# Optimization experiments

Measured on AMD Instinct MI355X. Metric: run time of the kernel, lower is better.

## Reference

```python
import jax, jax.numpy as jnp
import numpy as np

E = 8        # num_experts (material buckets)
L1 = 3072    # input dim
L2 = 15
L3 = 32
RF = 32      # ROUTER_FEATURES_PER_PERSPECTIVE
B = 16384
AUX_ALPHA = 0.01
Z_ALPHA = 0.001
LOAD_FLOOR = 0.05
LOAD_CAP = 0.5
PROBE_ALPHA = 0.01
PROBE_TAU = 1.0
PROBE_THRESH = 0.05
TEACHER_ALPHA = 0.0   # initial value of _teacher_alpha buffer
SCORE_SCALE = 600.0
SQ_SCALE = 255.0 / 256.0


def setup_inputs() -> dict:
    key = jax.random.key(0)
    ks = jax.random.split(key, 12)
    x = jax.random.uniform(ks[0], (B, L1), dtype=jnp.float32)
    ls_indices = jax.random.randint(ks[1], (B,), 0, E)
    psqt = jax.random.normal(ks[2], (B,), dtype=jnp.float32)
    score_target = jax.random.normal(ks[3], (B,), dtype=jnp.float32)
    router_w = 0.1 * jax.random.normal(ks[4], (E, 2 * RF), dtype=jnp.float32)
    router_b = jnp.zeros((E,), dtype=jnp.float32)
    # effective (coalesced) expert params, per _expert_params view
    w1 = jax.random.normal(ks[5], (E, L2 + 1, L1), dtype=jnp.float32) / np.sqrt(L1)
    b1 = 0.01 * jax.random.normal(ks[6], (E, L2 + 1), dtype=jnp.float32)
    w2 = jax.random.normal(ks[7], (E, L3, 2 * L2), dtype=jnp.float32) / np.sqrt(2 * L2)
    b2 = 0.01 * jax.random.normal(ks[8], (E, L3), dtype=jnp.float32)
    w3 = jax.random.normal(ks[9], (E, 1, L3), dtype=jnp.float32) / np.sqrt(L3)
    b3 = jnp.zeros((E, 1), dtype=jnp.float32)  # output bias zeroed in __init__
    return {"x": x, "ls_indices": ls_indices, "psqt": psqt,
            "score_target": score_target, "router_w": router_w,
            "router_b": router_b, "w1": w1, "b1": b1, "w2": w2, "b2": b2,
            "w3": w3, "b3": b3}


def _forward(x, psqt, score_target, router_w, router_b, w1, b1, w2, b2, w3, b3, ls_indices):
    half = L1 // 2
    router_in = jnp.concatenate([x[:, :RF], x[:, half:half + RF]], axis=1)  # [B, 64]
    gate_logits = router_in @ router_w.T + router_b                          # [B, E]
    logp = jax.nn.log_softmax(gate_logits, axis=-1)
    gate_probs = jnp.exp(logp)
    expert_indices = jnp.argmax(gate_logits, axis=-1)                        # [B]

    teacher_ce = -jnp.mean(jnp.take_along_axis(logp, ls_indices[:, None], axis=1))
    frac = jnp.bincount(expert_indices, length=E).astype(gate_probs.dtype) / gate_probs.shape[0]
    avg_gate = gate_probs.mean(axis=0)
    load = avg_gate + jax.lax.stop_gradient(frac - avg_gate)
    floor_loss = jnp.mean(jnp.square(jnp.maximum(LOAD_FLOOR - load, 0.0)))
    cap_loss = jnp.mean(jnp.square(jnp.maximum(load - LOAD_CAP, 0.0)))
    aux_loss = floor_loss + cap_loss
    z_loss = jnp.mean(jnp.square(jax.nn.logsumexp(gate_logits, axis=-1)))

    # ---- all-experts stacked MLP (fusion target) ----
    l1c = jnp.einsum('bi,eoi->beo', x, w1) + b1          # [B, E, L2+1]
    a, a_skip = l1c[..., :L2], l1c[..., L2:]              # [B,E,L2], [B,E,1]
    h = jnp.clip(jnp.concatenate([a * a * SQ_SCALE, a], axis=-1), 0.0, 1.0)  # [B,E,2*L2]
    l2x = jnp.clip(jnp.einsum('bei,eoi->beo', h, w2) + b2, 0.0, 1.0)         # [B,E,L3]
    all_out = jnp.einsum('bei,eoi->beo', l2x, w3) + b3 + a_skip              # [B,E,1]

    # ---- probe loss ----
    probe_weight = PROBE_ALPHA * max(PROBE_THRESH - TEACHER_ALPHA, 0.0) / max(PROBE_THRESH, 1e-9)
    expert_out = (all_out[..., 0] + psqt[:, None]) * SCORE_SCALE             # [B, E]
    err = jnp.square(expert_out - score_target[:, None])
    err = err - err.min(axis=1, keepdims=True)
    pt = jax.nn.softmax(-jax.lax.stop_gradient(err) / PROBE_TAU, axis=-1)
    log_pt = jnp.log(jnp.maximum(pt, 1e-30))
    probe_loss = jnp.mean(jnp.sum(pt * (log_pt - logp), axis=-1))            # kl_div batchmean

    router_loss = (AUX_ALPHA * aux_loss + Z_ALPHA * z_loss
                   + TEACHER_ALPHA * teacher_ce + probe_weight * probe_loss)

    l3x = jnp.take_along_axis(all_out, expert_indices[:, None, None], axis=1)[:, 0, :]  # [B, 1]
    gp = jnp.take_along_axis(gate_probs, expert_indices[:, None], axis=1)               # [B, 1]
    l3x = l3x * (1.0 + gp - jax.lax.stop_gradient(gp))  # straight-through (training mode)
    return l3x, router_loss


def reference(x, ls_indices, psqt, score_target, router_w, router_b, w1, b1, w2, b2, w3, b3):
    return _forward(x, psqt, score_target, router_w, router_b, w1, b1, w2, b2, w3, b3, ls_indices)
```

## Files before the change

### kernel.cpp

```cpp
#include <hip/hip_runtime.h>
#include <math.h>

#define BATCH 16384
#define K_DIM 3072
#define NEXP  8

typedef float  f32x4  __attribute__((ext_vector_type(4)));
typedef __bf16 bf16x8 __attribute__((ext_vector_type(8)));
typedef unsigned int u32x4 __attribute__((ext_vector_type(4)));
typedef unsigned int u32x2 __attribute__((ext_vector_type(2)));

__device__ __forceinline__ unsigned short f2bf(float f) {
  union { float f; unsigned u; } v; v.f = f;
  unsigned u = v.u + 0x7fffu + ((v.u >> 16) & 1u);
  return (unsigned short)(u >> 16);
}

__global__ void cvt_kernel(const float* __restrict__ w1, unsigned short* __restrict__ o,
                           const float* __restrict__ w2, float* __restrict__ w2t) {
  if (blockIdx.x < 384) {
    int i = blockIdx.x * 256 + threadIdx.x;
    f32x4 v = ((const f32x4*)w1)[i];
    u32x2 p = { (unsigned)f2bf(v.x) | ((unsigned)f2bf(v.y) << 16),
                (unsigned)f2bf(v.z) | ((unsigned)f2bf(v.w) << 16) };
    ((u32x2*)o)[i] = p;
  } else {
    for (int j = threadIdx.x; j < 7680; j += 256) {
      int e = j / 960; int r = j - e * 960; int oo = r / 30; int ii = r - oo * 30;
      w2t[e * 960 + ii * 32 + oo] = w2[j];
    }
  }
}

__global__ __launch_bounds__(256, 3) void moe_main_kernel(
    const float* __restrict__ x, const unsigned short* __restrict__ w1bf,
    const float* __restrict__ b1, const float* __restrict__ w2t,
    const float* __restrict__ b2, const float* __restrict__ w3,
    const float* __restrict__ b3, const float* __restrict__ psqt,
    const float* __restrict__ st, const float* __restrict__ rw,
    const float* __restrict__ rb, float* __restrict__ out,
    float* __restrict__ accs) {
  __shared__ __align__(16) unsigned short stage[32 * 72 + 128 * 72];
  __shared__ float rws_s[512];
  __shared__ float logps[32][8];
  __shared__ int   eidx_s[32];
  __shared__ int   hist_s[8];
  __shared__ float zsum_s;
  __shared__ float wred[4];

  const int tid = threadIdx.x;
  const int bm  = blockIdx.x;
  unsigned short* xs  = stage;
  unsigned short* wsd = stage + 32 * 72;
  float* Cl = (float*)stage;

  const int lane = tid & 63, wv = tid >> 6;
  const int l16 = lane & 15, lq = lane >> 4;
  const int rt = wv & 1;
  const int cb = (wv >> 1) * 4;

  const int xr0 = tid >> 4, xc4 = tid & 15;
  const float* gx0 = x + (size_t)(bm * 32 + xr0) * K_DIM + xc4 * 4;
  const float* gx1 = gx0 + (size_t)16 * K_DIM;
  const int xo0 = xr0 * 72 + xc4 * 4;
  const int xo1 = (xr0 + 16) * 72 + xc4 * 4;
  const int wr0 = tid >> 3, wc8 = tid & 7;
  const unsigned short* gw = w1bf + (size_t)wr0 * K_DIM + wc8 * 8;
  const int wo0 = wr0 * 72 + wc8 * 8;

  f32x4 xv0 = *(const f32x4*)gx0;
  f32x4 xv1 = *(const f32x4*)gx1;
  u32x4 wv0 = *(const u32x4*)(gw);
  u32x4 wv1 = *(const u32x4*)(gw + 32 * K_DIM);
  u32x4 wv2 = *(const u32x4*)(gw + 64 * K_DIM);
  u32x4 wv3 = *(const u32x4*)(gw + 96 * K_DIM);

  rws_s[tid] = rw[tid];
  rws_s[tid + 256] = rw[tid + 256];
  if (tid < 8) hist_s[tid] = 0;
  if (tid == 0) zsum_s = 0.f;
  __syncthreads();

  {
    const int rrow = tid >> 3, re = tid & 7;
    const float* xrow = x + (size_t)(bm * 32 + rrow) * K_DIM;
    double l = (double)rb[re];
#pragma unroll
    for (int c = 0; c < 32; ++c)
      l = fma((double)xrow[c], (double)rws_s[re * 64 + c], l);
#pragma unroll
    for (int c = 0; c < 32; ++c)
      l = fma((double)xrow[1536 + c], (double)rws_s[re * 64 + 32 + c], l);
    double mx = l;
    mx = fmax(mx, __shfl_xor(mx, 1));
    mx = fmax(mx, __shfl_xor(mx, 2));
    mx = fmax(mx, __shfl_xor(mx, 4));
    int cand = (l == mx) ? re : 8;
    cand = min(cand, __shfl_xor(cand, 1));
    cand = min(cand, __shfl_xor(cand, 2));
    cand = min(cand, __shfl_xor(cand, 4));
    double s = exp(l - mx);
    s += __shfl_xor(s, 1); s += __shfl_xor(s, 2); s += __shfl_xor(s, 4);
    double lse = mx + log(s);
    logps[rrow][re] = (float)(l - lse);
    if (re == 0) {
      eidx_s[rrow] = cand;
      atomicAdd(&zsum_s, (float)(lse * lse));
    }
    if (re == cand) atomicAdd(&hist_s[cand], 1);
  }

  f32x4 acc[4];
#pragma unroll
  for (int c = 0; c < 4; ++c) acc[c] = (f32x4){0.f, 0.f, 0.f, 0.f};

  const int abase = (rt * 16 + l16) * 72 + lq * 8;
  const int bbase = (cb * 16 + l16) * 72 + lq * 8;

  for (int kt = 0; kt < 48; ++kt) {
    __syncthreads();
    {
      u32x2 p0 = { (unsigned)f2bf(xv0.x) | ((unsigned)f2bf(xv0.y) << 16),
                   (unsigned)f2bf(xv0.z) | ((unsigned)f2bf(xv0.w) << 16) };
      *(u32x2*)&xs[xo0] = p0;
      u32x2 p1 = { (unsigned)f2bf(xv1.x) | ((unsigned)f2bf(xv1.y) << 16),
                   (unsigned)f2bf(xv1.z) | ((unsigned)f2bf(xv1.w) << 16) };
      *(u32x2*)&xs[xo1] = p1;
      *(u32x4*)&wsd[wo0]           = wv0;
      *(u32x4*)&wsd[wo0 + 32 * 72] = wv1;
      *(u32x4*)&wsd[wo0 + 64 * 72] = wv2;
      *(u32x4*)&wsd[wo0 + 96 * 72] = wv3;
    }
    __syncthreads();
    if (kt < 47) {
      gx0 += 64; gx1 += 64;
      xv0 = *(const f32x4*)gx0;
      xv1 = *(const f32x4*)gx1;
      const unsigned short* g = gw + (kt + 1) * 64;
      wv0 = *(const u32x4*)(g);
      wv1 = *(const u32x4*)(g + 32 * K_DIM);
      wv2 = *(const u32x4*)(g + 64 * K_DIM);
      wv3 = *(const u32x4*)(g + 96 * K_DIM);
    }
#pragma unroll
    for (int ks = 0; ks < 2; ++ks) {
      bf16x8 af = *(const bf16x8*)&xs[abase + ks * 32];
#pragma unroll
      for (int c = 0; c < 4; ++c) {
        bf16x8 bfv = *(const bf16x8*)&wsd[bbase + c * 16 * 72 + ks * 32];
        acc[c] = __builtin_amdgcn_mfma_f32_16x16x32_bf16(af, bfv, acc[c], 0, 0, 0);
      }
    }
  }

  __syncthreads();
#pragma unroll
  for (int c = 0; c < 4; ++c)
#pragma unroll
    for (int r = 0; r < 4; ++r)
      Cl[(rt * 16 + lq * 4 + r) * 132 + (cb + c) * 16 + l16] = acc[c][r];
  __syncthreads();

  const int bl = tid >> 3, e = tid & 7;
  const int bg = bm * 32 + bl;

  float a[16];
#pragma unroll
  for (int j = 0; j < 16; ++j) a[j] = Cl[bl * 132 + e * 16 + j] + b1[e * 16 + j];

  float h[30];
#pragma unroll
  for (int j = 0; j < 15; ++j) {
    float v = a[j];
    h[j]      = fminf(fmaxf(v * v * (255.0f / 256.0f), 0.f), 1.f);
    h[15 + j] = fminf(fmaxf(v, 0.f), 1.f);
  }

  float acc2[32];
  const f32x4* b2v = (const f32x4*)(b2 + e * 32);
#pragma unroll
  for (int o4 = 0; o4 < 8; ++o4) {
    f32x4 bq = b2v[o4];
    acc2[o4 * 4 + 0] = bq.x; acc2[o4 * 4 + 1] = bq.y;
    acc2[o4 * 4 + 2] = bq.z; acc2[o4 * 4 + 3] = bq.w;
  }
  const f32x4* wrow = (const f32x4*)(w2t + e * 960);
#pragma unroll
  for (int i = 0; i < 30; ++i) {
    float hv = h[i];
#pragma unroll
    for (int o4 = 0; o4 < 8; ++o4) {
      f32x4 wq = wrow[i * 8 + o4];
      acc2[o4 * 4 + 0] += hv * wq.x;
      acc2[o4 * 4 + 1] += hv * wq.y;
      acc2[o4 * 4 + 2] += hv * wq.z;
      acc2[o4 * 4 + 3] += hv * wq.w;
    }
  }

  float outv = b3[e] + a[15];
  const f32x4* w3v = (const f32x4*)(w3 + e * 32);
#pragma unroll
  for (int o4 = 0; o4 < 8; ++o4) {
    f32x4 wq = w3v[o4];
#pragma unroll
    for (int k = 0; k < 4; ++k) {
      float l2v = fminf(fmaxf(acc2[o4 * 4 + k], 0.f), 1.f);
      outv += l2v * ((const float*)&wq)[k];
    }
  }

  float eo  = (outv + psqt[bg]) * 600.0f;
  float dd  = eo - st[bg];
  float err = dd * dd;
  float mn = err;
  mn = fminf(mn, __shfl_xor(mn, 1));
  mn = fminf(mn, __shfl_xor(mn, 2));
  mn = fminf(mn, __shfl_xor(mn, 4));
  float wexp = expf(-(err - mn));
  float ssum = wexp;
  ssum += __shfl_xor(ssum, 1); ssum += __shfl_xor(ssum, 2); ssum += __shfl_xor(ssum, 4);
  float pt  = wexp / ssum;
  float lpt = logf(fmaxf(pt, 1e-30f));
  float term = pt * (lpt - logps[bl][e]);
  term += __shfl_xor(term, 1); term += __shfl_xor(term, 2); term += __shfl_xor(term, 4);
  float c1 = (e == 0) ? term : 0.f;
  c1 += __shfl_xor(c1, 8); c1 += __shfl_xor(c1, 16); c1 += __shfl_xor(c1, 32);
  if (lane == 0) wred[wv] = c1;

  if (e == eidx_s[bl]) out[bg] = outv;

  __syncthreads();
  if (tid == 0) {
    atomicAdd(&accs[9], wred[0] + wred[1] + wred[2] + wred[3]);
    atomicAdd(&accs[8], zsum_s);
  }
  if (tid < 8) atomicAdd(&accs[tid], (float)hist_s[tid]);
}

__global__ void finalize_kernel(const float* __restrict__ accs, float* __restrict__ out) {
  if (threadIdx.x == 0) {
    float fsum = 0.f;
    for (int e = 0; e < 8; ++e) {
      float frac = accs[e] * (1.0f / 16384.0f);
      float f = fmaxf(0.05f - frac, 0.f);
      float c = fmaxf(frac - 0.5f, 0.f);
      fsum += f * f + c * c;
    }
    float aux   = fsum * 0.125f;
    float z     = accs[8] * (1.0f / 16384.0f);
    float probe = accs[9] * (1.0f / 16384.0f);
    out[BATCH] = 0.01f * aux + 0.001f * z + 0.01f * probe;
  }
}

extern "C" void kernel_launch(void* const* d_in, const int* in_sizes, int n_in,
                              void* d_out, int out_size, void* d_ws, size_t ws_size,
                              hipStream_t stream) {
  const float* x    = (const float*)d_in[0];
  const float* psqt = (const float*)d_in[2];
  const float* st   = (const float*)d_in[3];
  const float* rw   = (const float*)d_in[4];
  const float* rb   = (const float*)d_in[5];
  const float* w1   = (const float*)d_in[6];
  const float* b1   = (const float*)d_in[7];
  const float* w2   = (const float*)d_in[8];
  const float* b2   = (const float*)d_in[9];
  const float* w3   = (const float*)d_in[10];
  const float* b3   = (const float*)d_in[11];
  float* out = (float*)d_out;

  unsigned short* w1bf = (unsigned short*)d_ws;
  float* w2t  = (float*)((char*)d_ws + 786432);
  float* accs = (float*)((char*)d_ws + 786432 + 30720);

  hipMemsetAsync(accs, 0, 16 * sizeof(float), stream);
  cvt_kernel<<<385, 256, 0, stream>>>(w1, w1bf, w2, w2t);
  moe_main_kernel<<<512, 256, 0, stream>>>(x, w1bf, b1, w2t, b2, w3, b3,
                                           psqt, st, rw, rb, out, accs);
  finalize_kernel<<<1, 1, 0, stream>>>(accs, out);
}
```

Measured before the change: 386.3 us.

## Split first-layer GEMM into split-K partial kernel and separate tail kernel

The fused kernel is split in two. A GEMM kernel uses 64-row tiles and a 3-way split along K, giving 768 blocks that each write fp32 partial sums to workspace. A separate tail kernel sums the partials, adds the bias, and runs the router, the small MLP layers and the losses. The aim is more parallelism and better reuse of the weight tiles across rows during the memory-bound read of x. The cost is an extra 3×16384×128 fp32 round trip through global memory plus one more kernel launch.

```diff
diff --git a/kernel.cpp b/kernel.cpp
--- a/kernel.cpp
+++ b/kernel.cpp
@@ -3,7 +3,10 @@
 
 #define BATCH 16384
 #define K_DIM 3072
-#define NEXP  8
+#define KS    3
+#define KSLICE 1024
+#define BM    64
+#define NITER 16
 
 typedef float  f32x4  __attribute__((ext_vector_type(4)));
 typedef __bf16 bf16x8 __attribute__((ext_vector_type(8)));
@@ -32,141 +35,156 @@
   }
 }
 
-__global__ __launch_bounds__(256, 3) void moe_main_kernel(
+__global__ __launch_bounds__(256, 3) void gemm_partial_kernel(
     const float* __restrict__ x, const unsigned short* __restrict__ w1bf,
+    float* __restrict__ partial) {
+  __shared__ __align__(16) unsigned short xs[64 * 72];
+  __shared__ __align__(16) unsigned short wsd[128 * 72];
+
+  const int tid = threadIdx.x;
+  const int bm  = blockIdx.x / KS;
+  const int ksl = blockIdx.x - bm * KS;
+  const int m0  = bm * BM;
+  const size_t k0 = (size_t)ksl * KSLICE;
+
+  const int srow = tid >> 4;
+  const int sc   = tid & 15;
+  const float*          gx = x    + (size_t)(m0 + srow) * K_DIM + k0 + sc * 4;
+  const unsigned short* gw = w1bf + (size_t)srow * K_DIM + k0 + sc * 4;
+  const int sxo = srow * 72 + sc * 4;
+
+  const int lane = tid & 63, wid = tid >> 6;
+  const int m16 = lane & 15, q = lane >> 4;
+  const int arow = (wid & 1) * 32;
+  const int bcol = (wid >> 1) * 64;
+
+  f32x4 acc[2][4];
+#pragma unroll
+  for (int i = 0; i < 2; ++i)
+#pragma unroll
+    for (int j = 0; j < 4; ++j) acc[i][j] = (f32x4){0.f, 0.f, 0.f, 0.f};
+
+  f32x4 xv[4];
+  u32x2 wv[8];
+#pragma unroll
+  for (int p = 0; p < 4; ++p) xv[p] = *(const f32x4*)(gx + (size_t)p * 16 * K_DIM);
+#pragma unroll
+  for (int p = 0; p < 8; ++p) wv[p] = *(const u32x2*)(gw + (size_t)p * 16 * K_DIM);
+
+  for (int kt = 0; kt < NITER; ++kt) {
+    __syncthreads();
+#pragma unroll
+    for (int p = 0; p < 4; ++p) {
+      u32x2 pk = { (unsigned)f2bf(xv[p].x) | ((unsigned)f2bf(xv[p].y) << 16),
+                   (unsigned)f2bf(xv[p].z) | ((unsigned)f2bf(xv[p].w) << 16) };
+      *(u32x2*)&xs[sxo + p * 16 * 72] = pk;
+    }
+#pragma unroll
+    for (int p = 0; p < 8; ++p)
+      *(u32x2*)&wsd[sxo + p * 16 * 72] = wv[p];
+    __syncthreads();
+    if (kt < NITER - 1) {
+      const size_t ko = (size_t)(kt + 1) * 64;
+#pragma unroll
+      for (int p = 0; p < 4; ++p) xv[p] = *(const f32x4*)(gx + (size_t)p * 16 * K_DIM + ko);
+#pragma unroll
+      for (int p = 0; p < 8; ++p) wv[p] = *(const u32x2*)(gw + (size_t)p * 16 * K_DIM + ko);
+    }
+#pragma unroll
+    for (int ks2 = 0; ks2 < 2; ++ks2) {
+      bf16x8 af[2];
+#pragma unroll
+      for (int i = 0; i < 2; ++i)
+        af[i] = *(const bf16x8*)&xs[(arow + i * 16 + m16) * 72 + ks2 * 32 + q * 8];
+#pragma unroll
+      for (int j = 0; j < 4; ++j) {
+        bf16x8 bf = *(const bf16x8*)&wsd[(bcol + j * 16 + m16) * 72 + ks2 * 32 + q * 8];
+#pragma unroll
+        for (int i = 0; i < 2; ++i)
+          acc[i][j] = __builtin_amdgcn_mfma_f32_16x16x32_bf16(af[i], bf, acc[i][j], 0, 0, 0);
+      }
+    }
+  }
+
+  float* pb = partial + (size_t)ksl * (BATCH * 128);
+#pragma unroll
+  for (int i = 0; i < 2; ++i)
+#pragma unroll
+    for (int j = 0; j < 4; ++j)
+#pragma unroll
+      for (int r = 0; r < 4; ++r)
+        pb[(size_t)(m0 + arow + i * 16 + q * 4 + r) * 128 + bcol + j * 16 + m16] = acc[i][j][r];
+}
+
+__global__ __launch_bounds__(256, 4) void moe_tail_kernel(
+    const float* __restrict__ x, const float* __restrict__ partial,
     const float* __restrict__ b1, const float* __restrict__ w2t,
     const float* __restrict__ b2, const float* __restrict__ w3,
     const float* __restrict__ b3, const float* __restrict__ psqt,
     const float* __restrict__ st, const float* __restrict__ rw,
     const float* __restrict__ rb, float* __restrict__ out,
     float* __restrict__ accs) {
-  __shared__ __align__(16) unsigned short stage[32 * 72 + 128 * 72];
   __shared__ float rws_s[512];
-  __shared__ float logps[32][8];
-  __shared__ int   eidx_s[32];
   __shared__ int   hist_s[8];
-  __shared__ float zsum_s;
-  __shared__ float wred[4];
+  __shared__ float zsum_s, psum_s;
 
   const int tid = threadIdx.x;
   const int bm  = blockIdx.x;
-  unsigned short* xs  = stage;
-  unsigned short* wsd = stage + 32 * 72;
-  float* Cl = (float*)stage;
-
-  const int lane = tid & 63, wv = tid >> 6;
-  const int l16 = lane & 15, lq = lane >> 4;
-  const int rt = wv & 1;
-  const int cb = (wv >> 1) * 4;
-
-  const int xr0 = tid >> 4, xc4 = tid & 15;
-  const float* gx0 = x + (size_t)(bm * 32 + xr0) * K_DIM + xc4 * 4;
-  const float* gx1 = gx0 + (size_t)16 * K_DIM;
-  const int xo0 = xr0 * 72 + xc4 * 4;
-  const int xo1 = (xr0 + 16) * 72 + xc4 * 4;
-  const int wr0 = tid >> 3, wc8 = tid & 7;
-  const unsigned short* gw = w1bf + (size_t)wr0 * K_DIM + wc8 * 8;
-  const int wo0 = wr0 * 72 + wc8 * 8;
-
-  f32x4 xv0 = *(const f32x4*)gx0;
-  f32x4 xv1 = *(const f32x4*)gx1;
-  u32x4 wv0 = *(const u32x4*)(gw);
-  u32x4 wv1 = *(const u32x4*)(gw + 32 * K_DIM);
-  u32x4 wv2 = *(const u32x4*)(gw + 64 * K_DIM);
-  u32x4 wv3 = *(const u32x4*)(gw + 96 * K_DIM);
-
   rws_s[tid] = rw[tid];
   rws_s[tid + 256] = rw[tid + 256];
   if (tid < 8) hist_s[tid] = 0;
-  if (tid == 0) zsum_s = 0.f;
+  if (tid == 0) { zsum_s = 0.f; psum_s = 0.f; }
   __syncthreads();
 
+  const int r = tid >> 3, e = tid & 7;
+  const int bg = bm * 32 + r;
+  const int lane = tid & 63, wid = tid >> 6;
+
+  float a[16];
   {
-    const int rrow = tid >> 3, re = tid & 7;
-    const float* xrow = x + (size_t)(bm * 32 + rrow) * K_DIM;
-    double l = (double)rb[re];
-#pragma unroll
-    for (int c = 0; c < 32; ++c)
-      l = fma((double)xrow[c], (double)rws_s[re * 64 + c], l);
-#pragma unroll
-    for (int c = 0; c < 32; ++c)
-      l = fma((double)xrow[1536 + c], (double)rws_s[re * 64 + 32 + c], l);
+    const size_t off = (size_t)bg * 128 + e * 16;
+#pragma unroll
+    for (int j4 = 0; j4 < 4; ++j4) {
+      f32x4 s = *(const f32x4*)(partial + off + j4 * 4);
+      s = s + *(const f32x4*)(partial + (size_t)BATCH * 128 + off + j4 * 4);
+      s = s + *(const f32x4*)(partial + (size_t)2 * BATCH * 128 + off + j4 * 4);
+      f32x4 bq = *(const f32x4*)(b1 + e * 16 + j4 * 4);
+      s = s + bq;
+      a[j4 * 4 + 0] = s.x; a[j4 * 4 + 1] = s.y; a[j4 * 4 + 2] = s.z; a[j4 * 4 + 3] = s.w;
+    }
+  }
+
+  float logp_own; int cand;
+  {
+    const float* xrow = x + (size_t)bg * K_DIM;
+    double l0 = (double)rb[e], l1 = 0.0;
+#pragma unroll
+    for (int c = 0; c < 32; c += 2) {
+      l0 = fma((double)xrow[c],     (double)rws_s[e * 64 + c],     l0);
+      l1 = fma((double)xrow[c + 1], (double)rws_s[e * 64 + c + 1], l1);
+    }
+#pragma unroll
+    for (int c = 0; c < 32; c += 2) {
+      l0 = fma((double)xrow[1536 + c],     (double)rws_s[e * 64 + 32 + c],     l0);
+      l1 = fma((double)xrow[1536 + c + 1], (double)rws_s[e * 64 + 32 + c + 1], l1);
+    }
+    double l = l0 + l1;
     double mx = l;
     mx = fmax(mx, __shfl_xor(mx, 1));
     mx = fmax(mx, __shfl_xor(mx, 2));
     mx = fmax(mx, __shfl_xor(mx, 4));
-    int cand = (l == mx) ? re : 8;
-    cand = min(cand, __shfl_xor(cand, 1));
-    cand = min(cand, __shfl_xor(cand, 2));
-    cand = min(cand, __shfl_xor(cand, 4));
+    int cd = (l == mx) ? e : 8;
+    cd = min(cd, __shfl_xor(cd, 1));
+    cd = min(cd, __shfl_xor(cd, 2));
+    cd = min(cd, __shfl_xor(cd, 4));
+    cand = cd;
     double s = exp(l - mx);
     s += __shfl_xor(s, 1); s += __shfl_xor(s, 2); s += __shfl_xor(s, 4);
     double lse = mx + log(s);
-    logps[rrow][re] = (float)(l - lse);
-    if (re == 0) {
-      eidx_s[rrow] = cand;
-      atomicAdd(&zsum_s, (float)(lse * lse));
-    }
-    if (re == cand) atomicAdd(&hist_s[cand], 1);
-  }
-
-  f32x4 acc[4];
-#pragma unroll
-  for (int c = 0; c < 4; ++c) acc[c] = (f32x4){0.f, 0.f, 0.f, 0.f};
-
-  const int abase = (rt * 16 + l16) * 72 + lq * 8;
-  const int bbase = (cb * 16 + l16) * 72 + lq * 8;
-
-  for (int kt = 0; kt < 48; ++kt) {
-    __syncthreads();
-    {
-      u32x2 p0 = { (unsigned)f2bf(xv0.x) | ((unsigned)f2bf(xv0.y) << 16),
-                   (unsigned)f2bf(xv0.z) | ((unsigned)f2bf(xv0.w) << 16) };
-      *(u32x2*)&xs[xo0] = p0;
-      u32x2 p1 = { (unsigned)f2bf(xv1.x) | ((unsigned)f2bf(xv1.y) << 16),
-                   (unsigned)f2bf(xv1.z) | ((unsigned)f2bf(xv1.w) << 16) };
-      *(u32x2*)&xs[xo1] = p1;
-      *(u32x4*)&wsd[wo0]           = wv0;
-      *(u32x4*)&wsd[wo0 + 32 * 72] = wv1;
-      *(u32x4*)&wsd[wo0 + 64 * 72] = wv2;
-      *(u32x4*)&wsd[wo0 + 96 * 72] = wv3;
-    }
-    __syncthreads();
-    if (kt < 47) {
-      gx0 += 64; gx1 += 64;
-      xv0 = *(const f32x4*)gx0;
-      xv1 = *(const f32x4*)gx1;
-      const unsigned short* g = gw + (kt + 1) * 64;
-      wv0 = *(const u32x4*)(g);
-      wv1 = *(const u32x4*)(g + 32 * K_DIM);
-      wv2 = *(const u32x4*)(g + 64 * K_DIM);
-      wv3 = *(const u32x4*)(g + 96 * K_DIM);
-    }
-#pragma unroll
-    for (int ks = 0; ks < 2; ++ks) {
-      bf16x8 af = *(const bf16x8*)&xs[abase + ks * 32];
-#pragma unroll
-      for (int c = 0; c < 4; ++c) {
-        bf16x8 bfv = *(const bf16x8*)&wsd[bbase + c * 16 * 72 + ks * 32];
-        acc[c] = __builtin_amdgcn_mfma_f32_16x16x32_bf16(af, bfv, acc[c], 0, 0, 0);
-      }
-    }
-  }
-
-  __syncthreads();
-#pragma unroll
-  for (int c = 0; c < 4; ++c)
-#pragma unroll
-    for (int r = 0; r < 4; ++r)
-      Cl[(rt * 16 + lq * 4 + r) * 132 + (cb + c) * 16 + l16] = acc[c][r];
-  __syncthreads();
-
-  const int bl = tid >> 3, e = tid & 7;
-  const int bg = bm * 32 + bl;
-
-  float a[16];
-#pragma unroll
-  for (int j = 0; j < 16; ++j) a[j] = Cl[bl * 132 + e * 16 + j] + b1[e * 16 + j];
+    logp_own = (float)(l - lse);
+    if (e == 0) atomicAdd(&zsum_s, (float)(lse * lse));
+    if (e == cd) atomicAdd(&hist_s[cd], 1);
+  }
 
   float h[30];
 #pragma unroll
@@ -222,18 +240,18 @@
   ssum += __shfl_xor(ssum, 1); ssum += __shfl_xor(ssum, 2); ssum += __shfl_xor(ssum, 4);
   float pt  = wexp / ssum;
   float lpt = logf(fmaxf(pt, 1e-30f));
-  float term = pt * (lpt - logps[bl][e]);
+  float term = pt * (lpt - logp_own);
   term += __shfl_xor(term, 1); term += __shfl_xor(term, 2); term += __shfl_xor(term, 4);
   float c1 = (e == 0) ? term : 0.f;
   c1 += __shfl_xor(c1, 8); c1 += __shfl_xor(c1, 16); c1 += __shfl_xor(c1, 32);
-  if (lane == 0) wred[wv] = c1;
-
-  if (e == eidx_s[bl]) out[bg] = outv;
+  if (lane == 0) atomicAdd(&psum_s, c1);
+
+  if (e == cand) out[bg] = outv;
 
   __syncthreads();
   if (tid == 0) {
-    atomicAdd(&accs[9], wred[0] + wred[1] + wred[2] + wred[3]);
     atomicAdd(&accs[8], zsum_s);
+    atomicAdd(&accs[9], psum_s);
   }
   if (tid < 8) atomicAdd(&accs[tid], (float)hist_s[tid]);
 }
@@ -271,12 +289,14 @@
   float* out = (float*)d_out;
 
   unsigned short* w1bf = (unsigned short*)d_ws;
-  float* w2t  = (float*)((char*)d_ws + 786432);
-  float* accs = (float*)((char*)d_ws + 786432 + 30720);
+  float* w2t     = (float*)((char*)d_ws + 786432);
+  float* accs    = (float*)((char*)d_ws + 786432 + 30720);
+  float* partial = (float*)((char*)d_ws + 1048576);
 
   hipMemsetAsync(accs, 0, 16 * sizeof(float), stream);
   cvt_kernel<<<385, 256, 0, stream>>>(w1, w1bf, w2, w2t);
-  moe_main_kernel<<<512, 256, 0, stream>>>(x, w1bf, b1, w2t, b2, w3, b3,
+  gemm_partial_kernel<<<768, 256, 0, stream>>>(x, w1bf, partial);
+  moe_tail_kernel<<<512, 256, 0, stream>>>(x, partial, b1, w2t, b2, w3, b3,
                                            psqt, st, rw, rb, out, accs);
   finalize_kernel<<<1, 1, 0, stream>>>(accs, out);
 }
```

Result: slower. 407.4 us (+5.4%).
